# Kernel optimization log

Hardware: AMD Instinct MI355X
Metric: run time of the kernel (lower is better)

Reference implementation:

```python
import jax, jax.numpy as jnp
import numpy as np


def _generate_linear_ibf(intervals, coeffs):
    # Faithful vectorization of generate_linear_ibf:
    # block i (i < n_vars): ones(n_vars,2); row i <- intervals[i]; row 0 *= coeffs[i]
    # block n_vars:         ones(n_vars,2); row 0 *= coeffs[n_vars]
    n_vars = intervals.shape[0]
    blocks = jnp.ones((n_vars + 1, n_vars, 2), dtype=coeffs.dtype)
    idx = jnp.arange(n_vars)
    blocks = blocks.at[idx, idx, :].set(intervals)            # set interval rows first
    blocks = blocks.at[:, 0, :].multiply(coeffs[:, None])     # then scale row 0 (matches torch order)
    return blocks.reshape((n_vars + 1) * n_vars, 2)


def setup_inputs() -> dict:
    key = jax.random.key(0)
    ks = jax.random.split(key, 6)
    n_vars, K = 4096, 4096
    return {
        "layer_inputs_under": jax.random.normal(ks[0], (K, n_vars + 1), dtype=jnp.float32),
        "layer_inputs_over": jax.random.normal(ks[1], (K, n_vars + 1), dtype=jnp.float32),
        "layer_inputs_under_degrees": jnp.ones((n_vars,), dtype=jnp.float32),
        "layer_inputs_over_degrees": jnp.ones((n_vars,), dtype=jnp.float32),
        "intervals": jax.random.uniform(ks[2], (n_vars, 2), dtype=jnp.float32),
        "node_pos_weights": jax.random.uniform(ks[3], (K,), dtype=jnp.float32),
        "node_neg_weights": -jax.random.uniform(ks[4], (K,), dtype=jnp.float32),
        "node_bias": jax.random.normal(ks[5], (1,), dtype=jnp.float32),
    }


def reference(layer_inputs_under, layer_inputs_over,
              layer_inputs_under_degrees, layer_inputs_over_degrees,
              intervals, node_pos_weights, node_neg_weights, node_bias):
    n_vars = intervals.shape[0]
    # ibf_tensor_prod_input_weights (generic nonzero path): (1,K) @ (K, n_vars+1)
    # NOTE: in torch, input_under[-1] += bias on a (1, n_vars+1) tensor adds the bias
    # to the entire (single) row; we reproduce that exactly.
    under_coeffs = (node_neg_weights @ layer_inputs_over
                    + node_pos_weights @ layer_inputs_under) + node_bias  # (n_vars+1,)
    over_coeffs = (node_pos_weights @ layer_inputs_over
                   + node_neg_weights @ layer_inputs_under) + node_bias   # (n_vars+1,)

    # degrees from both products are ones(n_vars); elementwise max is ones
    under_degree = jnp.ones((n_vars,), dtype=under_coeffs.dtype)
    over_degree = jnp.ones((n_vars,), dtype=over_coeffs.dtype)

    input_under = _generate_linear_ibf(intervals, under_coeffs)  # ((n_vars+1)*n_vars, 2)
    input_over = _generate_linear_ibf(intervals, over_coeffs)

    # activation == 'linear' branch
    return (input_under, input_over, under_degree, over_degree)
```

## Files before the change

### kernel.cpp

```cpp
#include <hip/hip_runtime.h>

#define TPB 256

__global__ __launch_bounds__(TPB) void fused_gemv_fill(
    const float* __restrict__ U, const float* __restrict__ O,
    const float* __restrict__ pos, const float* __restrict__ neg,
    const float* __restrict__ intervals,
    float* __restrict__ pu, float* __restrict__ po,
    float* __restrict__ outU, float* __restrict__ outO,
    int K, int ncols,
    int col_tiles, int rpc,
    int shift, int mask, int n4total, int n_gemv_blocks) {
  int b = blockIdx.x;

  if (b < n_gemv_blocks) {
    int tile  = b % col_tiles;
    int chunk = b / col_tiles;
    int j = tile * TPB + threadIdx.x;
    if (j >= ncols) return;
    int k0 = chunk * rpc;
    int k1 = k0 + rpc; if (k1 > K) k1 = K;

    const float* Uq = U + (size_t)k0 * ncols + j;
    const float* Oq = O + (size_t)k0 * ncols + j;
    const size_t st = (size_t)ncols;
    float au = 0.f, ao = 0.f;
    int k = k0;
    for (; k + 4 <= k1; k += 4) {
      float p0 = pos[k],   p1 = pos[k+1], p2 = pos[k+2], p3 = pos[k+3];
      float n0 = neg[k],   n1 = neg[k+1], n2 = neg[k+2], n3 = neg[k+3];
      float a0 = Uq[0], a1 = Uq[st], a2 = Uq[2*st], a3 = Uq[3*st];
      float b0 = Oq[0], b1 = Oq[st], b2 = Oq[2*st], b3 = Oq[3*st];
      Uq += 4*st; Oq += 4*st;
      au = fmaf(p0, a0, au); au = fmaf(n0, b0, au);
      ao = fmaf(p0, b0, ao); ao = fmaf(n0, a0, ao);
      au = fmaf(p1, a1, au); au = fmaf(n1, b1, au);
      ao = fmaf(p1, b1, ao); ao = fmaf(n1, a1, ao);
      au = fmaf(p2, a2, au); au = fmaf(n2, b2, au);
      ao = fmaf(p2, b2, ao); ao = fmaf(n2, a2, ao);
      au = fmaf(p3, a3, au); au = fmaf(n3, b3, au);
      ao = fmaf(p3, b3, ao); ao = fmaf(n3, a3, ao);
    }
    for (; k < k1; ++k) {
      float p = pos[k], n = neg[k];
      float a = Uq[0], bb = Oq[0];
      Uq += st; Oq += st;
      au = fmaf(p, a, au); au = fmaf(n, bb, au);
      ao = fmaf(p, bb, ao); ao = fmaf(n, a, ao);
    }
    pu[(size_t)chunk * ncols + j] = au;
    po[(size_t)chunk * ncols + j] = ao;
    return;
  }

  int i4 = (b - n_gemv_blocks) * TPB + threadIdx.x;
  if (i4 >= n4total) return;
  int i = i4 << 2;
  int blk = i >> shift;
  int within = i & mask;
  int r0 = within >> 1;

  float4 v = make_float4(1.f, 1.f, 1.f, 1.f);
  if (r0 == blk) {
    v.x = intervals[2 * blk];
    v.y = intervals[2 * blk + 1];
  } else if (r0 + 1 == blk) {
    v.z = intervals[2 * blk];
    v.w = intervals[2 * blk + 1];
  }
  reinterpret_cast<float4*>(outU)[i4] = v;
  reinterpret_cast<float4*>(outO)[i4] = v;
}

__global__ __launch_bounds__(TPB) void fill_scalar(
    const float* __restrict__ intervals,
    float* __restrict__ outU, float* __restrict__ outO,
    int n_vars, long long S) {
  long long tid = (long long)blockIdx.x * blockDim.x + threadIdx.x;
  long long nthreads = (long long)gridDim.x * blockDim.x;
  int two_n = 2 * n_vars;
  for (long long i = tid; i < S; i += nthreads) {
    int blk = (int)(i / two_n);
    int within = (int)(i - (long long)blk * two_n);
    int r = within >> 1;
    int c = within & 1;
    float v = 1.f;
    if (r == blk) v = intervals[2 * r + c];
    outU[i] = v;
    outO[i] = v;
  }
}

__global__ __launch_bounds__(TPB) void finish(
    const float* __restrict__ pu, const float* __restrict__ po,
    const float* __restrict__ intervals, const float* __restrict__ bias_p,
    float* __restrict__ outU, float* __restrict__ outO,
    float* __restrict__ degs,
    int ncols, int n_vars, int nchunks) {
  int t = blockIdx.x * TPB + threadIdx.x;
  int two_n = 2 * n_vars;
  if (t < two_n) degs[t] = 1.0f;

  if (t < ncols) {
    float s = bias_p[0];
    for (int c = 0; c < nchunks; ++c) s += pu[(size_t)c * ncols + t];
    float vx = s, vy = s;
    if (t == 0) { vx = intervals[0] * s; vy = intervals[1] * s; }
    size_t off = (size_t)t * two_n;
    outU[off] = vx; outU[off + 1] = vy;
  } else if (t < 2 * ncols) {
    int j = t - ncols;
    float s = bias_p[0];
    for (int c = 0; c < nchunks; ++c) s += po[(size_t)c * ncols + j];
    float vx = s, vy = s;
    if (j == 0) { vx = intervals[0] * s; vy = intervals[1] * s; }
    size_t off = (size_t)j * two_n;
    outO[off] = vx; outO[off + 1] = vy;
  }
}

extern "C" void kernel_launch(void* const* d_in, const int* in_sizes, int n_in,
                              void* d_out, int out_size, void* d_ws, size_t ws_size,
                              hipStream_t stream) {
  const float* U         = (const float*)d_in[0];
  const float* O         = (const float*)d_in[1];
  const float* intervals = (const float*)d_in[4];
  const float* pos       = (const float*)d_in[5];
  const float* neg       = (const float*)d_in[6];
  const float* bias      = (const float*)d_in[7];

  const int n_vars = in_sizes[4] / 2;
  const int K      = in_sizes[5];
  const int ncols  = n_vars + 1;

  int nchunks = 32;
  while (nchunks > 1 && (size_t)2 * nchunks * ncols * sizeof(float) > ws_size)
    nchunks >>= 1;
  float* pu = (float*)d_ws;
  float* po = pu + (size_t)nchunks * ncols;

  const int col_tiles = (ncols + TPB - 1) / TPB;
  const int rpc = (K + nchunks - 1) / nchunks;
  const int n_gemv_blocks = col_tiles * nchunks;

  const long long S = (long long)ncols * n_vars * 2;
  float* outU = (float*)d_out;
  float* outO = outU + S;
  float* degs = outU + 2 * S;

  const int two_n = 2 * n_vars;
  const bool pow2 = two_n > 0 && (two_n & (two_n - 1)) == 0;

  if (pow2 && S / 4 < (1LL << 31)) {
    int shift = __builtin_ctz((unsigned)two_n);
    int n4 = (int)(S / 4);
    int fill_blocks = (n4 + TPB - 1) / TPB;
    int grid = n_gemv_blocks + fill_blocks;
    fused_gemv_fill<<<grid, TPB, 0, stream>>>(
        U, O, pos, neg, intervals, pu, po, outU, outO,
        K, ncols, col_tiles, rpc, shift, two_n - 1, n4, n_gemv_blocks);
  } else {
    fused_gemv_fill<<<n_gemv_blocks, TPB, 0, stream>>>(
        U, O, pos, neg, intervals, pu, po, outU, outO,
        K, ncols, col_tiles, rpc, 0, 0, 0, n_gemv_blocks);
    fill_scalar<<<4096, TPB, 0, stream>>>(intervals, outU, outO, n_vars, S);
  }

  int nB = (2 * ncols > two_n ? 2 * ncols : two_n);
  finish<<<(nB + TPB - 1) / TPB, TPB, 0, stream>>>(
      pu, po, intervals, bias, outU, outO, degs, ncols, n_vars, nchunks);
}
```

Measured before the change: 386.4 us.

## Split GEMV into vectorized kernel and fuse reduction into fill pass

The GEMV moves into its own kernel that loads four columns per thread with float4 loads, uses 128 K-chunks instead of 32, and handles leftover columns in a scalar tail tile. The partial-sum reduction, bias add and interval scaling now happen inside the float4 fill kernel, which removes the separate strided `finish` pass over the outputs. Partial-sum rows are padded to a multiple of 8. In exchange, the fill no longer overlaps with the GEMV in a shared grid. Because ncols is odd, the float4 loads from U and O are misaligned rows, which may cost load efficiency.

Result: slower. 433.6 us (+12.2%).

```diff
diff --git a/kernel.cpp b/kernel.cpp
--- a/kernel.cpp
+++ b/kernel.cpp
@@ -2,59 +2,89 @@
 
 #define TPB 256
 
-__global__ __launch_bounds__(TPB) void fused_gemv_fill(
+__global__ __launch_bounds__(TPB) void gemv_vec(
     const float* __restrict__ U, const float* __restrict__ O,
     const float* __restrict__ pos, const float* __restrict__ neg,
-    const float* __restrict__ intervals,
     float* __restrict__ pu, float* __restrict__ po,
-    float* __restrict__ outU, float* __restrict__ outO,
-    int K, int ncols,
-    int col_tiles, int rpc,
-    int shift, int mask, int n4total, int n_gemv_blocks) {
-  int b = blockIdx.x;
-
-  if (b < n_gemv_blocks) {
-    int tile  = b % col_tiles;
-    int chunk = b / col_tiles;
-    int j = tile * TPB + threadIdx.x;
-    if (j >= ncols) return;
-    int k0 = chunk * rpc;
-    int k1 = k0 + rpc; if (k1 > K) k1 = K;
-
-    const float* Uq = U + (size_t)k0 * ncols + j;
-    const float* Oq = O + (size_t)k0 * ncols + j;
-    const size_t st = (size_t)ncols;
-    float au = 0.f, ao = 0.f;
+    int K, int ncols, int ps, int vec_tiles, int rpc) {
+  const int tiles_total = vec_tiles + 1;
+  const int chunk = blockIdx.x / tiles_total;
+  const int tile  = blockIdx.x % tiles_total;
+  const int k0 = chunk * rpc;
+  int k1 = k0 + rpc; if (k1 > K) k1 = K;
+
+  if (tile < vec_tiles) {
+    const int j = (tile * TPB + threadIdx.x) * 4;
+    float4 au = make_float4(0.f, 0.f, 0.f, 0.f);
+    float4 ao = make_float4(0.f, 0.f, 0.f, 0.f);
+    const float* Ub = U + j;
+    const float* Ob = O + j;
     int k = k0;
     for (; k + 4 <= k1; k += 4) {
-      float p0 = pos[k],   p1 = pos[k+1], p2 = pos[k+2], p3 = pos[k+3];
-      float n0 = neg[k],   n1 = neg[k+1], n2 = neg[k+2], n3 = neg[k+3];
-      float a0 = Uq[0], a1 = Uq[st], a2 = Uq[2*st], a3 = Uq[3*st];
-      float b0 = Oq[0], b1 = Oq[st], b2 = Oq[2*st], b3 = Oq[3*st];
-      Uq += 4*st; Oq += 4*st;
-      au = fmaf(p0, a0, au); au = fmaf(n0, b0, au);
-      ao = fmaf(p0, b0, ao); ao = fmaf(n0, a0, ao);
-      au = fmaf(p1, a1, au); au = fmaf(n1, b1, au);
-      ao = fmaf(p1, b1, ao); ao = fmaf(n1, a1, ao);
-      au = fmaf(p2, a2, au); au = fmaf(n2, b2, au);
-      ao = fmaf(p2, b2, ao); ao = fmaf(n2, a2, ao);
-      au = fmaf(p3, a3, au); au = fmaf(n3, b3, au);
-      ao = fmaf(p3, b3, ao); ao = fmaf(n3, a3, ao);
+      float p[4], n[4];
+      float4 a[4], b[4];
+#pragma unroll
+      for (int u = 0; u < 4; ++u) {
+        p[u] = pos[k + u];
+        n[u] = neg[k + u];
+        a[u] = *reinterpret_cast<const float4*>(Ub + (size_t)(k + u) * ncols);
+        b[u] = *reinterpret_cast<const float4*>(Ob + (size_t)(k + u) * ncols);
+      }
+#pragma unroll
+      for (int u = 0; u < 4; ++u) {
+        au.x = fmaf(p[u], a[u].x, au.x); au.y = fmaf(p[u], a[u].y, au.y);
+        au.z = fmaf(p[u], a[u].z, au.z); au.w = fmaf(p[u], a[u].w, au.w);
+        au.x = fmaf(n[u], b[u].x, au.x); au.y = fmaf(n[u], b[u].y, au.y);
+        au.z = fmaf(n[u], b[u].z, au.z); au.w = fmaf(n[u], b[u].w, au.w);
+        ao.x = fmaf(p[u], b[u].x, ao.x); ao.y = fmaf(p[u], b[u].y, ao.y);
+        ao.z = fmaf(p[u], b[u].z, ao.z); ao.w = fmaf(p[u], b[u].w, ao.w);
+        ao.x = fmaf(n[u], a[u].x, ao.x); ao.y = fmaf(n[u], a[u].y, ao.y);
+        ao.z = fmaf(n[u], a[u].z, ao.z); ao.w = fmaf(n[u], a[u].w, ao.w);
+      }
     }
     for (; k < k1; ++k) {
       float p = pos[k], n = neg[k];
-      float a = Uq[0], bb = Oq[0];
-      Uq += st; Oq += st;
-      au = fmaf(p, a, au); au = fmaf(n, bb, au);
-      ao = fmaf(p, bb, ao); ao = fmaf(n, a, ao);
-    }
-    pu[(size_t)chunk * ncols + j] = au;
-    po[(size_t)chunk * ncols + j] = ao;
-    return;
-  }
-
-  int i4 = (b - n_gemv_blocks) * TPB + threadIdx.x;
+      float4 a = *reinterpret_cast<const float4*>(Ub + (size_t)k * ncols);
+      float4 b = *reinterpret_cast<const float4*>(Ob + (size_t)k * ncols);
+      au.x = fmaf(p, a.x, au.x); au.y = fmaf(p, a.y, au.y);
+      au.z = fmaf(p, a.z, au.z); au.w = fmaf(p, a.w, au.w);
+      au.x = fmaf(n, b.x, au.x); au.y = fmaf(n, b.y, au.y);
+      au.z = fmaf(n, b.z, au.z); au.w = fmaf(n, b.w, au.w);
+      ao.x = fmaf(p, b.x, ao.x); ao.y = fmaf(p, b.y, ao.y);
+      ao.z = fmaf(p, b.z, ao.z); ao.w = fmaf(p, b.w, ao.w);
+      ao.x = fmaf(n, a.x, ao.x); ao.y = fmaf(n, a.y, ao.y);
+      ao.z = fmaf(n, a.z, ao.z); ao.w = fmaf(n, a.w, ao.w);
+    }
+    *reinterpret_cast<float4*>(pu + (size_t)chunk * ps + j) = au;
+    *reinterpret_cast<float4*>(po + (size_t)chunk * ps + j) = ao;
+  } else {
+    for (int j = vec_tiles * TPB * 4 + threadIdx.x; j < ncols; j += TPB) {
+      float au = 0.f, ao = 0.f;
+#pragma unroll 4
+      for (int k = k0; k < k1; ++k) {
+        float p = pos[k], n = neg[k];
+        float a = U[(size_t)k * ncols + j];
+        float b = O[(size_t)k * ncols + j];
+        au = fmaf(p, a, au); au = fmaf(n, b, au);
+        ao = fmaf(p, b, ao); ao = fmaf(n, a, ao);
+      }
+      pu[(size_t)chunk * ps + j] = au;
+      po[(size_t)chunk * ps + j] = ao;
+    }
+  }
+}
+
+__global__ __launch_bounds__(TPB) void fill_finish(
+    const float* __restrict__ intervals,
+    const float* __restrict__ pu, const float* __restrict__ po,
+    const float* __restrict__ bias_p,
+    float* __restrict__ outU, float* __restrict__ outO,
+    float* __restrict__ degs,
+    int n_vars, int shift, int mask, int n4total, int nchunks, int ps) {
+  int i4 = blockIdx.x * TPB + threadIdx.x;
+  if (i4 < 2 * n_vars) degs[i4] = 1.0f;
   if (i4 >= n4total) return;
+
   int i = i4 << 2;
   int blk = i >> shift;
   int within = i & mask;
@@ -68,8 +98,22 @@
     v.z = intervals[2 * blk];
     v.w = intervals[2 * blk + 1];
   }
-  reinterpret_cast<float4*>(outU)[i4] = v;
-  reinterpret_cast<float4*>(outO)[i4] = v;
+
+  float4 vu = v, vo = v;
+  if (within == 0) {
+    float bb = bias_p[0];
+    float su = bb, so = bb;
+#pragma unroll 8
+    for (int c = 0; c < nchunks; ++c) {
+      su += pu[(size_t)c * ps + blk];
+      so += po[(size_t)c * ps + blk];
+    }
+    vu.x = v.x * su; vu.y = v.y * su;
+    vo.x = v.x * so; vo.y = v.y * so;
+  }
+
+  reinterpret_cast<float4*>(outU)[i4] = vu;
+  reinterpret_cast<float4*>(outO)[i4] = vo;
 }
 
 __global__ __launch_bounds__(TPB) void fill_scalar(
@@ -96,14 +140,13 @@
     const float* __restrict__ intervals, const float* __restrict__ bias_p,
     float* __restrict__ outU, float* __restrict__ outO,
     float* __restrict__ degs,
-    int ncols, int n_vars, int nchunks) {
+    int ncols, int n_vars, int nchunks, int ps) {
   int t = blockIdx.x * TPB + threadIdx.x;
   int two_n = 2 * n_vars;
   if (t < two_n) degs[t] = 1.0f;
-
   if (t < ncols) {
     float s = bias_p[0];
-    for (int c = 0; c < nchunks; ++c) s += pu[(size_t)c * ncols + t];
+    for (int c = 0; c < nchunks; ++c) s += pu[(size_t)c * ps + t];
     float vx = s, vy = s;
     if (t == 0) { vx = intervals[0] * s; vy = intervals[1] * s; }
     size_t off = (size_t)t * two_n;
@@ -111,7 +154,7 @@
   } else if (t < 2 * ncols) {
     int j = t - ncols;
     float s = bias_p[0];
-    for (int c = 0; c < nchunks; ++c) s += po[(size_t)c * ncols + j];
+    for (int c = 0; c < nchunks; ++c) s += po[(size_t)c * ps + j];
     float vx = s, vy = s;
     if (j == 0) { vx = intervals[0] * s; vy = intervals[1] * s; }
     size_t off = (size_t)j * two_n;
@@ -132,16 +175,19 @@
   const int n_vars = in_sizes[4] / 2;
   const int K      = in_sizes[5];
   const int ncols  = n_vars + 1;
-
-  int nchunks = 32;
-  while (nchunks > 1 && (size_t)2 * nchunks * ncols * sizeof(float) > ws_size)
+  const int ps     = (ncols + 7) & ~7;
+
+  int nchunks = 128;
+  while (nchunks > 1 && (size_t)2 * nchunks * ps * sizeof(float) > ws_size)
     nchunks >>= 1;
+  const int rpc = (K + nchunks - 1) / nchunks;
   float* pu = (float*)d_ws;
-  float* po = pu + (size_t)nchunks * ncols;
-
-  const int col_tiles = (ncols + TPB - 1) / TPB;
-  const int rpc = (K + nchunks - 1) / nchunks;
-  const int n_gemv_blocks = col_tiles * nchunks;
+  float* po = pu + (size_t)nchunks * ps;
+
+  const int vec_tiles = ncols / (TPB * 4);
+
+  gemv_vec<<<nchunks * (vec_tiles + 1), TPB, 0, stream>>>(
+      U, O, pos, neg, pu, po, K, ncols, ps, vec_tiles, rpc);
 
   const long long S = (long long)ncols * n_vars * 2;
   float* outU = (float*)d_out;
@@ -154,19 +200,15 @@
   if (pow2 && S / 4 < (1LL << 31)) {
     int shift = __builtin_ctz((unsigned)two_n);
     int n4 = (int)(S / 4);
-    int fill_blocks = (n4 + TPB - 1) / TPB;
-    int grid = n_gemv_blocks + fill_blocks;
-    fused_gemv_fill<<<grid, TPB, 0, stream>>>(
-        U, O, pos, neg, intervals, pu, po, outU, outO,
-        K, ncols, col_tiles, rpc, shift, two_n - 1, n4, n_gemv_blocks);
+    long long nthreads = n4 > two_n ? n4 : two_n;
+    int blocks = (int)((nthreads + TPB - 1) / TPB);
+    fill_finish<<<blocks, TPB, 0, stream>>>(
+        intervals, pu, po, bias, outU, outO, degs,
+        n_vars, shift, two_n - 1, n4, nchunks, ps);
   } else {
-    fused_gemv_fill<<<n_gemv_blocks, TPB, 0, stream>>>(
-        U, O, pos, neg, intervals, pu, po, outU, outO,
-        K, ncols, col_tiles, rpc, 0, 0, 0, n_gemv_blocks);
     fill_scalar<<<4096, TPB, 0, stream>>>(intervals, outU, outO, n_vars, S);
-  }
-
-  int nB = (2 * ncols > two_n ? 2 * ncols : two_n);
-  finish<<<(nB + TPB - 1) / TPB, TPB, 0, stream>>>(
-      pu, po, intervals, bias, outU, outO, degs, ncols, n_vars, nchunks);
-}
+    int nB = (2 * ncols > two_n ? 2 * ncols : two_n);
+    finish<<<(nB + TPB - 1) / TPB, TPB, 0, stream>>>(
+        pu, po, intervals, bias, outU, outO, degs, ncols, n_vars, nchunks, ps);
+  }
+}
```
